# Performance work log

Hardware: AMD Instinct MI355X
Metric: run time of the kernel (lower is better)

## Reference

```python
import jax, jax.numpy as jnp
import numpy as np

# Geometry of the single LocallyConnected2d layer being decomposed
FACTOR = 2      # number of sublayers the out_channels are split into
KH = KW = 3     # kernel size
DH = DW = 1     # stride
OH = OW = 32    # output spatial size
B, C_IN, C_OUT = 128, 32, 64
H = W = OH + KH - 1  # 34 (valid unfold with stride 1)


def setup_inputs() -> dict:
    key = jax.random.key(0)
    kx, kw_, kb = jax.random.split(key, 3)
    x = jax.random.normal(kx, (B, C_IN, H, W), dtype=jnp.float32)
    # per-location weights: (out_ch, in_ch, oh, ow, kh*kw) -- no weight sharing
    weight = jax.random.normal(kw_, (C_OUT, C_IN, OH, OW, KH * KW), dtype=jnp.float32) * 0.05
    bias = jax.random.normal(kb, (C_OUT, OH, OW), dtype=jnp.float32)
    return {"x": x, "weight": weight, "bias": bias}


def _unfold(x):
    # x: (B, C, H, W) -> patches: (B, C, OH, OW, KH*KW)
    # equivalent to torch x.unfold(2,kh,dh).unfold(3,kw,dw).reshape(..., kh*kw)
    cols = [x[:, :, i:i + DH * OH:DH, j:j + DW * OW:DW]
            for i in range(KH) for j in range(KW)]
    return jnp.stack(cols, axis=-1)


def reference(x, weight, bias):
    patches = _unfold(x)  # (B, C, OH, OW, K2)
    new_ch = weight.shape[0] // FACTOR
    outs = []
    for g in range(FACTOR):  # decomposed sublayers, concatenated on channel dim
        w_g = weight[g * new_ch:(g + 1) * new_ch]
        b_g = bias[g * new_ch:(g + 1) * new_ch]
        # out[b,o,i,j] = sum_{c,k} patches[b,c,i,j,k] * w[o,c,i,j,k] + b[o,i,j]
        o_g = jnp.einsum('bcijk,ocijk->boij', patches, w_g) + b_g[None]
        outs.append(o_g)
    return jnp.concatenate(outs, axis=1)  # (B, C_OUT, OH, OW)
```

## Files before the change

### kernel.cpp

```cpp
#include <hip/hip_runtime.h>
#include <cstdint>
#include <cstddef>

#define B_    128
#define C_    32
#define O_    64
#define H_    34
#define NPOS  1024
#define K9    9
#define BC    (B_ * C_)
#define BO    (B_ * O_)
#define P_    (O_ * C_)

typedef __bf16 v8bf __attribute__((ext_vector_type(8)));
typedef float  v4f  __attribute__((ext_vector_type(4)));
typedef float  f4u  __attribute__((ext_vector_type(4), aligned(4)));

__device__ __forceinline__ unsigned short f2bf(float f) {
    union { float f; unsigned int u; } v; v.f = f;
    unsigned int u = v.u;
    return (unsigned short)((u + 0x7FFFu + ((u >> 16) & 1u)) >> 16);
}
__device__ __forceinline__ float bf2f(unsigned short s) {
    union { unsigned int u; float f; } v; v.u = ((unsigned int)s) << 16;
    return v.f;
}

__global__ __launch_bounds__(256) void repack_x(const float* __restrict__ x,
                                                unsigned short* __restrict__ x2) {
    const int ph = blockIdx.x;
    const int b0 = (ph / H_) * 2;
    const int h  = ph % H_;
    __shared__ unsigned short tile[2][C_][H_ + 2];
    const int t = threadIdx.x;
    for (int e = t; e < 2 * C_ * H_; e += 256) {
        const int bb = e / (C_ * H_);
        const int rem = e % (C_ * H_);
        const int c = rem / H_, w = rem % H_;
        tile[bb][c][w] = f2bf(x[(((size_t)(b0 + bb) * C_ + c) * H_ + h) * H_ + w]);
    }
    __syncthreads();
    for (int e = t; e < H_ * 64; e += 256) {
        const int w = e >> 6;
        const int idx = e & 63;
        x2[((size_t)(h * H_ + w)) * BC + b0 * C_ + idx] = tile[idx >> 5][idx & 31][w];
    }
}

template <int MODE>
__global__ __launch_bounds__(256, 4) void lc_main(const float* __restrict__ x,
                                                  const unsigned short* __restrict__ x2,
                                                  const float* __restrict__ weight,
                                                  const float* __restrict__ bias,
                                                  void* __restrict__ dstv) {
    const int bid = blockIdx.x;
    const int pos = ((bid & 7) << 7) | (bid >> 3);
    const int i = pos >> 5, j = pos & 31;
    const int t  = threadIdx.x;
    const int wv = t >> 6;
    const int l  = t & 63;
    const int lm = l & 15;
    const int q  = l >> 4;

    float bv[4];
#pragma unroll
    for (int nt = 0; nt < 4; ++nt)
        bv[nt] = bias[(size_t)(nt * 16 + lm) * NPOS + pos];

    v4f acc[2][4];
#pragma unroll
    for (int a = 0; a < 2; ++a)
#pragma unroll
        for (int n = 0; n < 4; ++n) acc[a][n] = (v4f){0.f, 0.f, 0.f, 0.f};

    if constexpr (MODE == 1) {
        __shared__ __align__(16) unsigned short Wl[K9 * P_];
#pragma unroll
        for (int pp = 0; pp < 8; ++pp) {
            const int p = pp * 256 + t;
            const float* wp = weight + ((size_t)p * NPOS + pos) * K9;
            f4u w0 = *(const f4u*)wp;
            f4u w1 = *(const f4u*)(wp + 4);
            float w8 = wp[8];
            unsigned short s[9];
            s[0] = f2bf(w0[0]); s[1] = f2bf(w0[1]); s[2] = f2bf(w0[2]); s[3] = f2bf(w0[3]);
            s[4] = f2bf(w1[0]); s[5] = f2bf(w1[1]); s[6] = f2bf(w1[2]); s[7] = f2bf(w1[3]);
            s[8] = f2bf(w8);
#pragma unroll
            for (int k = 0; k < K9; ++k)
                Wl[k * P_ + p] = s[k];
        }
        __syncthreads();

        const unsigned short* xb = x2 + (size_t)(i * H_ + j) * BC;
#pragma unroll
        for (int k = 0; k < K9; ++k) {
            const int off = ((k / 3) * H_ + (k % 3)) * BC;
            v8bf af[2], bfr[4];
#pragma unroll
            for (int mt = 0; mt < 2; ++mt)
                af[mt] = *(const v8bf*)(xb + off + (wv * 32 + mt * 16 + lm) * C_ + q * 8);
#pragma unroll
            for (int nt = 0; nt < 4; ++nt)
                bfr[nt] = *(const v8bf*)&Wl[k * P_ + (nt * 16 + lm) * C_ + q * 8];
#pragma unroll
            for (int mt = 0; mt < 2; ++mt)
#pragma unroll
                for (int nt = 0; nt < 4; ++nt)
                    acc[mt][nt] = __builtin_amdgcn_mfma_f32_16x16x32_bf16(
                        af[mt], bfr[nt], acc[mt][nt], 0, 0, 0);
        }
    } else {
        for (int k = 0; k < K9; ++k) {
            const int kh = k / 3, kw = k % 3;
            v8bf af[2], bfr[4];
#pragma unroll
            for (int mt = 0; mt < 2; ++mt) {
                const int b = wv * 32 + mt * 16 + lm;
                union { v8bf v; unsigned short s[8]; } u;
#pragma unroll
                for (int cc = 0; cc < 8; ++cc)
                    u.s[cc] = f2bf(x[(((size_t)b * C_ + q * 8 + cc) * H_ + (i + kh)) * H_ + (j + kw)]);
                af[mt] = u.v;
            }
#pragma unroll
            for (int nt = 0; nt < 4; ++nt) {
                union { v8bf v; unsigned short s[8]; } u;
#pragma unroll
                for (int cc = 0; cc < 8; ++cc) {
                    const int p = (nt * 16 + lm) * C_ + q * 8 + cc;
                    u.s[cc] = f2bf(weight[((size_t)p * NPOS + pos) * K9 + k]);
                }
                bfr[nt] = u.v;
            }
#pragma unroll
            for (int mt = 0; mt < 2; ++mt)
#pragma unroll
                for (int nt = 0; nt < 4; ++nt)
                    acc[mt][nt] = __builtin_amdgcn_mfma_f32_16x16x32_bf16(
                        af[mt], bfr[nt], acc[mt][nt], 0, 0, 0);
        }
    }

    if constexpr (MODE == 1) {
        unsigned short* wsp = (unsigned short*)dstv + (size_t)pos * BO;
#pragma unroll
        for (int mt = 0; mt < 2; ++mt)
#pragma unroll
            for (int nt = 0; nt < 4; ++nt) {
                const int o = nt * 16 + lm;
#pragma unroll
                for (int r = 0; r < 4; ++r) {
                    const int b = wv * 32 + mt * 16 + q * 4 + r;
                    wsp[b * O_ + o] = f2bf(acc[mt][nt][r] + bv[nt]);
                }
            }
    } else {
        float* outp = (float*)dstv;
#pragma unroll
        for (int mt = 0; mt < 2; ++mt)
#pragma unroll
            for (int nt = 0; nt < 4; ++nt) {
                const int o = nt * 16 + lm;
#pragma unroll
                for (int r = 0; r < 4; ++r) {
                    const int b = wv * 32 + mt * 16 + q * 4 + r;
                    outp[(size_t)(b * O_ + o) * NPOS + pos] = acc[mt][nt][r] + bv[nt];
                }
            }
    }
}

__global__ __launch_bounds__(256) void transpose_out(const unsigned short* __restrict__ ws,
                                                     float* __restrict__ out) {
    __shared__ float tile[64][65];
    const int tb  = blockIdx.x;
    const int bo0 = (tb >> 4) * 64;
    const int p0  = (tb & 15) * 64;
    const int tx  = threadIdx.x & 63;
    const int ty  = threadIdx.x >> 6;
#pragma unroll
    for (int r = 0; r < 16; ++r)
        tile[r * 4 + ty][tx] = bf2f(ws[(size_t)(p0 + r * 4 + ty) * BO + bo0 + tx]);
    __syncthreads();
#pragma unroll
    for (int r = 0; r < 16; ++r)
        out[(size_t)(bo0 + r * 4 + ty) * NPOS + p0 + tx] = tile[tx][r * 4 + ty];
}

extern "C" void kernel_launch(void* const* d_in, const int* in_sizes, int n_in,
                              void* d_out, int out_size, void* d_ws, size_t ws_size,
                              hipStream_t stream) {
    const float* x      = (const float*)d_in[0];
    const float* weight = (const float*)d_in[1];
    const float* bias   = (const float*)d_in[2];
    float* out          = (float*)d_out;

    const size_t WSB = (size_t)NPOS * BO * sizeof(unsigned short);
    const size_t X2B = (size_t)H_ * H_ * BC * sizeof(unsigned short);

    if (ws_size >= WSB + X2B) {
        unsigned short* wsout = (unsigned short*)d_ws;
        unsigned short* x2 = (unsigned short*)((char*)d_ws + WSB);
        repack_x<<<(B_ / 2) * H_, 256, 0, stream>>>(x, x2);
        lc_main<1><<<NPOS, 256, 0, stream>>>(x, x2, weight, bias, wsout);
        transpose_out<<<2048, 256, 0, stream>>>(wsout, out);
    } else {
        lc_main<0><<<NPOS, 256, 0, stream>>>(x, nullptr, weight, bias, out);
    }
}
```

Baseline: 175.2 us.

## Retile main kernel over 4 adjacent positions and 16 outputs for coalesced weight loads

Each block of the main kernel now covers 4 consecutive output columns and 16 output channels instead of one position and all 64 channels. Because those 4 positions are contiguous in memory, the weight staging reads one contiguous run of 36 floats per (o,c) pair, replacing the previous strided 9-float gathers across positions. The workspace layout changes to pos-major with o before b, so accumulator stores become packed 4-wide bf16 writes, and the transpose kernel is reindexed to match. In exchange each block issues more MFMAs per weight fragment but reloads activation rows once per 16-channel group, which raises global traffic for x.

```diff
diff --git a/kernel.cpp b/kernel.cpp
--- a/kernel.cpp
+++ b/kernel.cpp
@@ -10,11 +10,10 @@
 #define K9    9
 #define BC    (B_ * C_)
 #define BO    (B_ * O_)
-#define P_    (O_ * C_)
 
 typedef __bf16 v8bf __attribute__((ext_vector_type(8)));
 typedef float  v4f  __attribute__((ext_vector_type(4)));
-typedef float  f4u  __attribute__((ext_vector_type(4), aligned(4)));
+typedef float  f2u  __attribute__((ext_vector_type(2), aligned(4)));
 
 __device__ __forceinline__ unsigned short f2bf(float f) {
     union { float f; unsigned int u; } v; v.f = f;
@@ -47,14 +46,83 @@
     }
 }
 
-template <int MODE>
-__global__ __launch_bounds__(256, 4) void lc_main(const float* __restrict__ x,
-                                                  const unsigned short* __restrict__ x2,
-                                                  const float* __restrict__ weight,
-                                                  const float* __restrict__ bias,
-                                                  void* __restrict__ dstv) {
+__global__ __launch_bounds__(256, 4) void lc_fused(const unsigned short* __restrict__ x2,
+                                                   const float* __restrict__ weight,
+                                                   const float* __restrict__ bias,
+                                                   unsigned short* __restrict__ ws) {
+    __shared__ __align__(16) unsigned short Wl[36 * 512];
+
     const int bid = blockIdx.x;
-    const int pos = ((bid & 7) << 7) | (bid >> 3);
+    const int jq = bid & 7;
+    const int i  = (bid >> 3) & 31;
+    const int oq = bid >> 8;
+    const int j0 = jq * 4;
+    const int o0 = oq * 16;
+    const int posbase = i * 32 + j0;
+    const int t = threadIdx.x;
+
+    const float* wbase = weight + ((size_t)(o0 * C_) * NPOS + posbase) * K9;
+#pragma unroll
+    for (int r = 0; r < 36; ++r) {
+        const int idx = r * 256 + t;
+        const int pl = idx / 18;
+        const int d2 = idx % 18;
+        const f2u v = *(const f2u*)(wbase + (size_t)pl * (NPOS * K9) + d2 * 2);
+        const int d = d2 * 2;
+        Wl[d * 512 + pl]       = f2bf(v[0]);
+        Wl[(d + 1) * 512 + pl] = f2bf(v[1]);
+    }
+    __syncthreads();
+
+    const int wv = t >> 6;
+    const int l  = t & 63;
+    const int lm = l & 15;
+    const int q  = l >> 4;
+
+    v4f acc[4][2];
+#pragma unroll
+    for (int a = 0; a < 4; ++a)
+#pragma unroll
+        for (int m = 0; m < 2; ++m) acc[a][m] = (v4f){0.f, 0.f, 0.f, 0.f};
+
+#pragma unroll
+    for (int tap = 0; tap < K9; ++tap) {
+        const int kh = tap / 3, kw = tap % 3;
+        const int rowbase = (i + kh) * H_ + j0 + kw;
+#pragma unroll
+        for (int jj = 0; jj < 4; ++jj) {
+            const v8bf bfr = *(const v8bf*)&Wl[(jj * K9 + tap) * 512 + lm * C_ + q * 8];
+            const unsigned short* xrow = x2 + (size_t)(rowbase + jj) * BC;
+            const v8bf af0 = *(const v8bf*)(xrow + (wv * 32 + lm) * C_ + q * 8);
+            const v8bf af1 = *(const v8bf*)(xrow + (wv * 32 + 16 + lm) * C_ + q * 8);
+            acc[jj][0] = __builtin_amdgcn_mfma_f32_16x16x32_bf16(af0, bfr, acc[jj][0], 0, 0, 0);
+            acc[jj][1] = __builtin_amdgcn_mfma_f32_16x16x32_bf16(af1, bfr, acc[jj][1], 0, 0, 0);
+        }
+    }
+
+#pragma unroll
+    for (int jj = 0; jj < 4; ++jj) {
+        const int pos = posbase + jj;
+        const float bv = bias[(size_t)(o0 + lm) * NPOS + pos];
+        unsigned short* wp = ws + (size_t)pos * BO + (o0 + lm) * B_;
+#pragma unroll
+        for (int mt = 0; mt < 2; ++mt) {
+            const int b = wv * 32 + mt * 16 + q * 4;
+            ushort4 pk;
+            pk.x = f2bf(acc[jj][mt][0] + bv);
+            pk.y = f2bf(acc[jj][mt][1] + bv);
+            pk.z = f2bf(acc[jj][mt][2] + bv);
+            pk.w = f2bf(acc[jj][mt][3] + bv);
+            *(ushort4*)(wp + b) = pk;
+        }
+    }
+}
+
+__global__ __launch_bounds__(256) void lc_fallback(const float* __restrict__ x,
+                                                   const float* __restrict__ weight,
+                                                   const float* __restrict__ bias,
+                                                   float* __restrict__ out) {
+    const int pos = blockIdx.x;
     const int i = pos >> 5, j = pos & 31;
     const int t  = threadIdx.x;
     const int wv = t >> 6;
@@ -73,119 +141,70 @@
 #pragma unroll
         for (int n = 0; n < 4; ++n) acc[a][n] = (v4f){0.f, 0.f, 0.f, 0.f};
 
-    if constexpr (MODE == 1) {
-        __shared__ __align__(16) unsigned short Wl[K9 * P_];
-#pragma unroll
-        for (int pp = 0; pp < 8; ++pp) {
-            const int p = pp * 256 + t;
-            const float* wp = weight + ((size_t)p * NPOS + pos) * K9;
-            f4u w0 = *(const f4u*)wp;
-            f4u w1 = *(const f4u*)(wp + 4);
-            float w8 = wp[8];
-            unsigned short s[9];
-            s[0] = f2bf(w0[0]); s[1] = f2bf(w0[1]); s[2] = f2bf(w0[2]); s[3] = f2bf(w0[3]);
-            s[4] = f2bf(w1[0]); s[5] = f2bf(w1[1]); s[6] = f2bf(w1[2]); s[7] = f2bf(w1[3]);
-            s[8] = f2bf(w8);
-#pragma unroll
-            for (int k = 0; k < K9; ++k)
-                Wl[k * P_ + p] = s[k];
-        }
-        __syncthreads();
-
-        const unsigned short* xb = x2 + (size_t)(i * H_ + j) * BC;
-#pragma unroll
-        for (int k = 0; k < K9; ++k) {
-            const int off = ((k / 3) * H_ + (k % 3)) * BC;
-            v8bf af[2], bfr[4];
-#pragma unroll
-            for (int mt = 0; mt < 2; ++mt)
-                af[mt] = *(const v8bf*)(xb + off + (wv * 32 + mt * 16 + lm) * C_ + q * 8);
+    for (int k = 0; k < K9; ++k) {
+        const int kh = k / 3, kw = k % 3;
+        v8bf af[2], bfr[4];
+#pragma unroll
+        for (int mt = 0; mt < 2; ++mt) {
+            const int b = wv * 32 + mt * 16 + lm;
+            union { v8bf v; unsigned short s[8]; } u;
+#pragma unroll
+            for (int cc = 0; cc < 8; ++cc)
+                u.s[cc] = f2bf(x[(((size_t)b * C_ + q * 8 + cc) * H_ + (i + kh)) * H_ + (j + kw)]);
+            af[mt] = u.v;
+        }
+#pragma unroll
+        for (int nt = 0; nt < 4; ++nt) {
+            union { v8bf v; unsigned short s[8]; } u;
+#pragma unroll
+            for (int cc = 0; cc < 8; ++cc) {
+                const int p = (nt * 16 + lm) * C_ + q * 8 + cc;
+                u.s[cc] = f2bf(weight[((size_t)p * NPOS + pos) * K9 + k]);
+            }
+            bfr[nt] = u.v;
+        }
+#pragma unroll
+        for (int mt = 0; mt < 2; ++mt)
 #pragma unroll
             for (int nt = 0; nt < 4; ++nt)
-                bfr[nt] = *(const v8bf*)&Wl[k * P_ + (nt * 16 + lm) * C_ + q * 8];
-#pragma unroll
-            for (int mt = 0; mt < 2; ++mt)
-#pragma unroll
-                for (int nt = 0; nt < 4; ++nt)
-                    acc[mt][nt] = __builtin_amdgcn_mfma_f32_16x16x32_bf16(
-                        af[mt], bfr[nt], acc[mt][nt], 0, 0, 0);
-        }
-    } else {
-        for (int k = 0; k < K9; ++k) {
-            const int kh = k / 3, kw = k % 3;
-            v8bf af[2], bfr[4];
-#pragma unroll
-            for (int mt = 0; mt < 2; ++mt) {
-                const int b = wv * 32 + mt * 16 + lm;
-                union { v8bf v; unsigned short s[8]; } u;
-#pragma unroll
-                for (int cc = 0; cc < 8; ++cc)
-                    u.s[cc] = f2bf(x[(((size_t)b * C_ + q * 8 + cc) * H_ + (i + kh)) * H_ + (j + kw)]);
-                af[mt] = u.v;
+                acc[mt][nt] = __builtin_amdgcn_mfma_f32_16x16x32_bf16(
+                    af[mt], bfr[nt], acc[mt][nt], 0, 0, 0);
+    }
+#pragma unroll
+    for (int mt = 0; mt < 2; ++mt)
+#pragma unroll
+        for (int nt = 0; nt < 4; ++nt) {
+            const int o = nt * 16 + lm;
+#pragma unroll
+            for (int r = 0; r < 4; ++r) {
+                const int b = wv * 32 + mt * 16 + q * 4 + r;
+                out[(size_t)(b * O_ + o) * NPOS + pos] = acc[mt][nt][r] + bv[nt];
             }
-#pragma unroll
-            for (int nt = 0; nt < 4; ++nt) {
-                union { v8bf v; unsigned short s[8]; } u;
-#pragma unroll
-                for (int cc = 0; cc < 8; ++cc) {
-                    const int p = (nt * 16 + lm) * C_ + q * 8 + cc;
-                    u.s[cc] = f2bf(weight[((size_t)p * NPOS + pos) * K9 + k]);
-                }
-                bfr[nt] = u.v;
-            }
-#pragma unroll
-            for (int mt = 0; mt < 2; ++mt)
-#pragma unroll
-                for (int nt = 0; nt < 4; ++nt)
-                    acc[mt][nt] = __builtin_amdgcn_mfma_f32_16x16x32_bf16(
-                        af[mt], bfr[nt], acc[mt][nt], 0, 0, 0);
-        }
-    }
-
-    if constexpr (MODE == 1) {
-        unsigned short* wsp = (unsigned short*)dstv + (size_t)pos * BO;
-#pragma unroll
-        for (int mt = 0; mt < 2; ++mt)
-#pragma unroll
-            for (int nt = 0; nt < 4; ++nt) {
-                const int o = nt * 16 + lm;
-#pragma unroll
-                for (int r = 0; r < 4; ++r) {
-                    const int b = wv * 32 + mt * 16 + q * 4 + r;
-                    wsp[b * O_ + o] = f2bf(acc[mt][nt][r] + bv[nt]);
-                }
-            }
-    } else {
-        float* outp = (float*)dstv;
-#pragma unroll
-        for (int mt = 0; mt < 2; ++mt)
-#pragma unroll
-            for (int nt = 0; nt < 4; ++nt) {
-                const int o = nt * 16 + lm;
-#pragma unroll
-                for (int r = 0; r < 4; ++r) {
-                    const int b = wv * 32 + mt * 16 + q * 4 + r;
-                    outp[(size_t)(b * O_ + o) * NPOS + pos] = acc[mt][nt][r] + bv[nt];
-                }
-            }
-    }
+        }
 }
 
 __global__ __launch_bounds__(256) void transpose_out(const unsigned short* __restrict__ ws,
                                                      float* __restrict__ out) {
     __shared__ float tile[64][65];
-    const int tb  = blockIdx.x;
-    const int bo0 = (tb >> 4) * 64;
-    const int p0  = (tb & 15) * 64;
-    const int tx  = threadIdx.x & 63;
-    const int ty  = threadIdx.x >> 6;
-#pragma unroll
-    for (int r = 0; r < 16; ++r)
-        tile[r * 4 + ty][tx] = bf2f(ws[(size_t)(p0 + r * 4 + ty) * BO + bo0 + tx]);
+    const int tb = blockIdx.x;
+    const int o  = tb >> 5;
+    const int bt = (tb >> 4) & 1;
+    const int pt = tb & 15;
+    const int b0 = bt * 64;
+    const int p0 = pt * 64;
+    const int tx = threadIdx.x & 63;
+    const int ty = threadIdx.x >> 6;
+#pragma unroll
+    for (int r = 0; r < 16; ++r) {
+        const int pr = r * 4 + ty;
+        tile[pr][tx] = bf2f(ws[(size_t)(p0 + pr) * BO + o * B_ + b0 + tx]);
+    }
     __syncthreads();
 #pragma unroll
-    for (int r = 0; r < 16; ++r)
-        out[(size_t)(bo0 + r * 4 + ty) * NPOS + p0 + tx] = tile[tx][r * 4 + ty];
+    for (int r = 0; r < 16; ++r) {
+        const int br = r * 4 + ty;
+        out[((size_t)(b0 + br) * O_ + o) * NPOS + p0 + tx] = tile[tx][br];
+    }
 }
 
 extern "C" void kernel_launch(void* const* d_in, const int* in_sizes, int n_in,
@@ -203,9 +222,9 @@
         unsigned short* wsout = (unsigned short*)d_ws;
         unsigned short* x2 = (unsigned short*)((char*)d_ws + WSB);
         repack_x<<<(B_ / 2) * H_, 256, 0, stream>>>(x, x2);
-        lc_main<1><<<NPOS, 256, 0, stream>>>(x, x2, weight, bias, wsout);
+        lc_fused<<<1024, 256, 0, stream>>>(x2, weight, bias, wsout);
         transpose_out<<<2048, 256, 0, stream>>>(wsout, out);
     } else {
-        lc_main<0><<<NPOS, 256, 0, stream>>>(x, nullptr, weight, bias, out);
-    }
-}
+        lc_fallback<<<NPOS, 256, 0, stream>>>(x, weight, bias, out);
+    }
+}
```

New measurement: 167.8 us. 1.04x faster.
